# Performance work log

Hardware: AMD Instinct MI355X
Metric: run time of the kernel (lower is better)

The kernel has to match this reference:

```python
import jax, jax.numpy as jnp
import numpy as np

K = 3  # kernel_size
PAD = 1


def _unfold3x3(x):
    # x: [b, c, h, w] -> patches [b, c, k*k, h, w] matching torch.nn.Unfold
    # ordering (row-major over the kernel window, channel outermost).
    b, c, h, w = x.shape
    xp = jnp.pad(x, ((0, 0), (0, 0), (PAD, PAD), (PAD, PAD)))
    patches = jnp.stack(
        [xp[:, :, i:i + h, j:j + w] for i in range(K) for j in range(K)],
        axis=2,
    )
    return patches  # [b, c, 9, h, w]


def setup_inputs() -> dict:
    key = jax.random.key(0)
    k1, k2, k3, k4 = jax.random.split(key, 4)
    b, c, h, w = 8, 64, 128, 128
    out_ch = 64
    x = jax.random.normal(k1, (b, c, h, w), dtype=jnp.float32)
    guide_ch = jax.random.normal(k2, (b, c, h, w), dtype=jnp.float32)
    guide_sp = jax.random.normal(k3, (b, K * K, h, w), dtype=jnp.float32)
    # kaiming_normal_ fan_out on [out, in, k^2, 1, 1]: fan_out = out * k^2 * 1 * 1?
    # torch fan_out for 5D conv weight = out_channels * receptive_field (k^2*1*1)
    fan_out = out_ch * (K * K)
    std = np.sqrt(2.0 / fan_out)
    weight = jax.random.normal(k4, (out_ch, c, K * K), dtype=jnp.float32) * std
    return {"x": x, "guide_ch": guide_ch, "guide_sp": guide_sp, "weight": weight}


def reference(x, guide_ch, guide_sp, weight):
    # filter: [b, c, k^2, h, w] = 1 + tanh(guide_ch[:, :, None] + guide_sp[:, None])
    filt = 1.0 + jnp.tanh(guide_ch[:, :, None, :, :] + guide_sp[:, None, :, :, :])
    patches = _unfold3x3(x)  # [b, c, 9, h, w]
    # conv3d with weight [out, in, k^2, 1, 1] == per-pixel reduction over (c, k^2)
    out = jnp.einsum('bckhw,ock->bohw', patches * filt, weight)
    return out
```

## Files before the change

### kernel.cpp

```cpp
#include <hip/hip_runtime.h>
#include <hip/hip_bf16.h>

typedef short short8 __attribute__((ext_vector_type(8)));
typedef float floatx4 __attribute__((ext_vector_type(4)));

#define HWSZ 16384
#define WD 128
#define CD 64
#define OD 64
#define XSTR 72
#define OSTR 132
#define L2E2 2.8853900817779268f

__device__ __forceinline__ short f2bf(float f) {
    unsigned u = __builtin_bit_cast(unsigned, f);
    u += 0x7FFFu + ((u >> 16) & 1u);
    return (short)(u >> 16);
}

__device__ __forceinline__ unsigned pack2bf(float a, float b) {
    __hip_bfloat162 h = __float22bfloat162_rn(float2{a, b});
    unsigned u;
    __builtin_memcpy(&u, &h, 4);
    return u;
}

__device__ __forceinline__ float bf2f(short s) {
    return __builtin_bit_cast(float, ((unsigned)(unsigned short)s) << 16);
}

__global__ void prepack_w(const float* __restrict__ wgt, unsigned short* __restrict__ wp) {
    int idx = blockIdx.x * 256 + threadIdx.x;
    if (idx < 9 * 64 * 64) {
        int k = idx >> 12, o = (idx >> 6) & 63, c = idx & 63;
        wp[idx] = (unsigned short)f2bf(wgt[o * 576 + c * 9 + k]);
    }
}

__global__ __launch_bounds__(256, 3)
void paka_kernel(const float* __restrict__ x, const float* __restrict__ gc,
                 const float* __restrict__ gs, const float* __restrict__ wgt,
                 const unsigned short* __restrict__ wp, float* __restrict__ out)
{
    __shared__ union {
        struct {
            short xl[130 * XSTR];
            short wl[3][64 * XSTR];
        } s;
        float o[64 * OSTR];
    } lds;

    const int tid  = threadIdx.x;
    const int wave = tid >> 6;
    const int lane = tid & 63;
    const int b = blockIdx.x >> 7;
    const int h = blockIdx.x & 127;

    const float* xb  = x  + (size_t)b * CD * HWSZ;
    const float* gcb = gc + (size_t)b * CD * HWSZ;
    const float* gsb = gs + (size_t)b * 9 * HWSZ;

    const int row = lane & 15;
    const int q   = lane >> 4;
    const int mt0 = wave * 2;

    float eg[2][2][8];
    #pragma unroll
    for (int mt = 0; mt < 2; ++mt) {
        int p = (mt0 + mt) * 16 + row;
        #pragma unroll
        for (int ks = 0; ks < 2; ++ks)
            #pragma unroll
            for (int j = 0; j < 8; ++j) {
                int c = ks * 32 + q * 8 + j;
                eg[mt][ks][j] = __builtin_amdgcn_exp2f(gcb[(size_t)c * HWSZ + h * WD + p] * L2E2);
            }
    }
    float esv[9][2];
    #pragma unroll
    for (int k = 0; k < 9; ++k)
        #pragma unroll
        for (int mt = 0; mt < 2; ++mt) {
            int p = (mt0 + mt) * 16 + row;
            esv[k][mt] = __builtin_amdgcn_exp2f(gsb[k * HWSZ + h * WD + p] * L2E2);
        }

    if (tid < 32)
        *(unsigned*)&lds.s.xl[0 * XSTR + tid * 2] = 0u;
    else if (tid < 64)
        *(unsigned*)&lds.s.xl[129 * XSTR + (tid - 32) * 2] = 0u;

    floatx4 acc[2][4];
    #pragma unroll
    for (int i = 0; i < 2; ++i)
        #pragma unroll
        for (int n = 0; n < 4; ++n)
            acc[i][n] = (floatx4){0.f, 0.f, 0.f, 0.f};

    #pragma unroll
    for (int dh = 0; dh < 3; ++dh) {
        const int hh = h + dh - 1;
        if ((unsigned)hh >= 128u) continue;

        __syncthreads();

        if (wp) {
            #pragma unroll
            for (int it = 0; it < 6; ++it) {
                int idx = it * 256 + tid;
                int dw = idx >> 9, o = (idx >> 3) & 63, cg = idx & 7;
                short8 v = *(const short8*)&wp[(dh * 3 + dw) * 4096 + o * 64 + cg * 8];
                *(short8*)&lds.s.wl[dw][o * XSTR + cg * 8] = v;
            }
        } else {
            #pragma unroll
            for (int it = 0; it < 48; ++it) {
                int idx = it * 256 + tid;
                int dw = idx >> 12, o = (idx >> 6) & 63, c = idx & 63;
                lds.s.wl[dw][o * XSTR + c] = f2bf(wgt[o * 576 + c * 9 + dh * 3 + dw]);
            }
        }

        #pragma unroll
        for (int it = 0; it < 4; ++it) {
            int idx = it * 256 + tid;
            int cp = idx >> 5;
            int p4 = (idx & 31) * 4;
            const float* x0 = xb + (size_t)(2 * cp) * HWSZ + hh * WD + p4;
            floatx4 a = *(const floatx4*)x0;
            floatx4 c4 = *(const floatx4*)(x0 + HWSZ);
            #pragma unroll
            for (int i = 0; i < 4; ++i)
                *(unsigned*)&lds.s.xl[(p4 + i + 1) * XSTR + 2 * cp] = pack2bf(a[i], c4[i]);
        }

        __syncthreads();

        #pragma unroll
        for (int dw = 0; dw < 3; ++dw) {
            const int k = dh * 3 + dw;
            #pragma unroll
            for (int ks = 0; ks < 2; ++ks) {
                short8 af[2];
                #pragma unroll
                for (int mt = 0; mt < 2; ++mt) {
                    int wslot = (mt0 + mt) * 16 + row + dw;
                    short8 raw = *(const short8*)&lds.s.xl[wslot * XSTR + ks * 32 + q * 8];
                    float es = esv[k][mt];
                    #pragma unroll
                    for (int jj = 0; jj < 4; ++jj) {
                        float d0 = fmaf(eg[mt][ks][2 * jj],     es, 1.0f);
                        float d1 = fmaf(eg[mt][ks][2 * jj + 1], es, 1.0f);
                        float r0 = __builtin_amdgcn_rcpf(d0);
                        float r1 = __builtin_amdgcn_rcpf(d1);
                        float x20 = bf2f(raw[2 * jj]);     x20 += x20;
                        float x21 = bf2f(raw[2 * jj + 1]); x21 += x21;
                        float t0 = fmaf(-x20, r0, x20);
                        float t1 = fmaf(-x21, r1, x21);
                        ((unsigned*)&af[mt])[jj] = pack2bf(t0, t1);
                    }
                }
                #pragma unroll
                for (int nt = 0; nt < 4; ++nt) {
                    short8 bv = *(const short8*)&lds.s.wl[dw][(nt * 16 + row) * XSTR + ks * 32 + q * 8];
                    acc[0][nt] = __builtin_amdgcn_mfma_f32_16x16x32_bf16(af[0], bv, acc[0][nt], 0, 0, 0);
                    acc[1][nt] = __builtin_amdgcn_mfma_f32_16x16x32_bf16(af[1], bv, acc[1][nt], 0, 0, 0);
                }
            }
        }
    }

    __syncthreads();

    #pragma unroll
    for (int i = 0; i < 2; ++i) {
        int prow = (mt0 + i) * 16 + q * 4;
        #pragma unroll
        for (int nt = 0; nt < 4; ++nt) {
            int o = nt * 16 + row;
            #pragma unroll
            for (int r = 0; r < 4; ++r)
                lds.o[o * OSTR + prow + r] = acc[i][nt][r];
        }
    }

    __syncthreads();

    float* outb = out + ((size_t)b * OD) * HWSZ + h * WD;
    #pragma unroll
    for (int it = 0; it < 8; ++it) {
        int idx = it * 256 + tid;
        int o = idx >> 5, p4 = (idx & 31) * 4;
        *(floatx4*)&outb[(size_t)o * HWSZ + p4] = *(const floatx4*)&lds.o[o * OSTR + p4];
    }
}

extern "C" void kernel_launch(void* const* d_in, const int* in_sizes, int n_in,
                              void* d_out, int out_size, void* d_ws, size_t ws_size,
                              hipStream_t stream) {
    const float* x   = (const float*)d_in[0];
    const float* gcp = (const float*)d_in[1];
    const float* gsp = (const float*)d_in[2];
    const float* wgt = (const float*)d_in[3];
    float* out = (float*)d_out;

    const bool use_wp = ws_size >= (size_t)(9 * 64 * 64 * sizeof(unsigned short));
    unsigned short* wp = use_wp ? (unsigned short*)d_ws : nullptr;
    if (use_wp)
        prepack_w<<<dim3(144), dim3(256), 0, stream>>>(wgt, wp);
    paka_kernel<<<dim3(1024), dim3(256), 0, stream>>>(x, gcp, gsp, wgt, wp, out);
}
```

Baseline: 145.9 us.

## Pre-transpose x to padded bf16 NHWC and read operands directly from global

Adds a separate kernel that converts each input row of x into a zero-padded, channel-contiguous bf16 layout in workspace. The main kernel then loads A and B MFMA fragments straight from global/L2 instead of staging them through LDS, which removes the per-row syncthreads and shrinks LDS so occupancy can rise to 4 blocks. The factor of 2 is folded into the prepacked weights, and the spatial exponentials are computed per kernel row. This costs an extra kernel launch and an extra round trip of x through memory (about 33MB read, 17MB written), and it only runs when the workspace is large enough; otherwise a fallback kernel is used.

```diff
diff --git a/kernel.cpp b/kernel.cpp
--- a/kernel.cpp
+++ b/kernel.cpp
@@ -3,13 +3,15 @@
 
 typedef short short8 __attribute__((ext_vector_type(8)));
 typedef float floatx4 __attribute__((ext_vector_type(4)));
+typedef unsigned uint4v __attribute__((ext_vector_type(4)));
 
 #define HWSZ 16384
 #define WD 128
 #define CD 64
 #define OD 64
-#define XSTR 72
 #define OSTR 132
+#define XTROW (130 * 64)
+#define WP_BYTES (9 * 64 * 64 * 2)
 #define L2E2 2.8853900817779268f
 
 __device__ __forceinline__ short f2bf(float f) {
@@ -33,22 +35,52 @@
     int idx = blockIdx.x * 256 + threadIdx.x;
     if (idx < 9 * 64 * 64) {
         int k = idx >> 12, o = (idx >> 6) & 63, c = idx & 63;
-        wp[idx] = (unsigned short)f2bf(wgt[o * 576 + c * 9 + k]);
-    }
-}
-
-__global__ __launch_bounds__(256, 3)
-void paka_kernel(const float* __restrict__ x, const float* __restrict__ gc,
-                 const float* __restrict__ gs, const float* __restrict__ wgt,
-                 const unsigned short* __restrict__ wp, float* __restrict__ out)
+        wp[idx] = (unsigned short)f2bf(2.0f * wgt[o * 576 + c * 9 + k]);
+    }
+}
+
+__global__ __launch_bounds__(256, 2)
+void transpose_x(const float* __restrict__ x, unsigned short* __restrict__ xt) {
+    __shared__ unsigned ld[128 * 33];
+    const int tid = threadIdx.x;
+    const int b = blockIdx.x >> 7;
+    const int h = blockIdx.x & 127;
+    const float* xr = x + (size_t)b * CD * HWSZ + h * WD;
+
+    #pragma unroll
+    for (int it = 0; it < 16; ++it) {
+        int idx = it * 256 + tid;
+        int cd = idx >> 7;
+        int w  = idx & 127;
+        float a  = xr[(size_t)(2 * cd) * HWSZ + w];
+        float b2 = xr[(size_t)(2 * cd + 1) * HWSZ + w];
+        ld[w * 33 + cd] = pack2bf(a, b2);
+    }
+    __syncthreads();
+
+    unsigned short* xo = xt + (size_t)(b * 128 + h) * XTROW;
+    if (tid < 16) {
+        int slot = (tid >> 3) ? 129 : 0;
+        int cq = tid & 7;
+        *(uint4v*)&xo[slot * 64 + cq * 8] = (uint4v){0u, 0u, 0u, 0u};
+    }
+    #pragma unroll
+    for (int it = 0; it < 4; ++it) {
+        int idx = it * 256 + tid;
+        int w = idx >> 3, cq = idx & 7;
+        uint4v v;
+        #pragma unroll
+        for (int i = 0; i < 4; ++i) v[i] = ld[w * 33 + cq * 4 + i];
+        *(uint4v*)&xo[(1 + w) * 64 + cq * 8] = v;
+    }
+}
+
+__global__ __launch_bounds__(256, 4)
+void paka_main(const float* __restrict__ gc, const float* __restrict__ gs,
+               const unsigned short* __restrict__ wp,
+               const unsigned short* __restrict__ xt, float* __restrict__ out)
 {
-    __shared__ union {
-        struct {
-            short xl[130 * XSTR];
-            short wl[3][64 * XSTR];
-        } s;
-        float o[64 * OSTR];
-    } lds;
+    __shared__ float lo[64 * OSTR];
 
     const int tid  = threadIdx.x;
     const int wave = tid >> 6;
@@ -56,7 +88,6 @@
     const int b = blockIdx.x >> 7;
     const int h = blockIdx.x & 127;
 
-    const float* xb  = x  + (size_t)b * CD * HWSZ;
     const float* gcb = gc + (size_t)b * CD * HWSZ;
     const float* gsb = gs + (size_t)b * 9 * HWSZ;
 
@@ -76,19 +107,6 @@
                 eg[mt][ks][j] = __builtin_amdgcn_exp2f(gcb[(size_t)c * HWSZ + h * WD + p] * L2E2);
             }
     }
-    float esv[9][2];
-    #pragma unroll
-    for (int k = 0; k < 9; ++k)
-        #pragma unroll
-        for (int mt = 0; mt < 2; ++mt) {
-            int p = (mt0 + mt) * 16 + row;
-            esv[k][mt] = __builtin_amdgcn_exp2f(gsb[k * HWSZ + h * WD + p] * L2E2);
-        }
-
-    if (tid < 32)
-        *(unsigned*)&lds.s.xl[0 * XSTR + tid * 2] = 0u;
-    else if (tid < 64)
-        *(unsigned*)&lds.s.xl[129 * XSTR + (tid - 32) * 2] = 0u;
 
     floatx4 acc[2][4];
     #pragma unroll
@@ -102,30 +120,138 @@
         const int hh = h + dh - 1;
         if ((unsigned)hh >= 128u) continue;
 
+        const unsigned short* xr = xt + (size_t)(b * 128 + hh) * XTROW;
+
+        float esd[3][2];
+        #pragma unroll
+        for (int dw = 0; dw < 3; ++dw)
+            #pragma unroll
+            for (int mt = 0; mt < 2; ++mt) {
+                int p = (mt0 + mt) * 16 + row;
+                esd[dw][mt] = __builtin_amdgcn_exp2f(gsb[(dh * 3 + dw) * HWSZ + h * WD + p] * L2E2);
+            }
+
+        #pragma unroll
+        for (int dw = 0; dw < 3; ++dw) {
+            const int k = dh * 3 + dw;
+            #pragma unroll
+            for (int ks = 0; ks < 2; ++ks) {
+                short8 raw[2];
+                #pragma unroll
+                for (int mt = 0; mt < 2; ++mt) {
+                    int wslot = (mt0 + mt) * 16 + row + dw;
+                    raw[mt] = *(const short8*)&xr[(size_t)wslot * 64 + ks * 32 + q * 8];
+                }
+                short8 bv[4];
+                #pragma unroll
+                for (int nt = 0; nt < 4; ++nt)
+                    bv[nt] = *(const short8*)&wp[k * 4096 + (nt * 16 + row) * 64 + ks * 32 + q * 8];
+
+                short8 af[2];
+                #pragma unroll
+                for (int mt = 0; mt < 2; ++mt) {
+                    float es = esd[dw][mt];
+                    #pragma unroll
+                    for (int jj = 0; jj < 4; ++jj) {
+                        float d0 = fmaf(eg[mt][ks][2 * jj],     es, 1.0f);
+                        float d1 = fmaf(eg[mt][ks][2 * jj + 1], es, 1.0f);
+                        float r0 = __builtin_amdgcn_rcpf(d0);
+                        float r1 = __builtin_amdgcn_rcpf(d1);
+                        float x0 = bf2f(raw[mt][2 * jj]);
+                        float x1 = bf2f(raw[mt][2 * jj + 1]);
+                        float t0 = fmaf(-x0, r0, x0);
+                        float t1 = fmaf(-x1, r1, x1);
+                        ((unsigned*)&af[mt])[jj] = pack2bf(t0, t1);
+                    }
+                }
+                #pragma unroll
+                for (int nt = 0; nt < 4; ++nt) {
+                    acc[0][nt] = __builtin_amdgcn_mfma_f32_16x16x32_bf16(af[0], bv[nt], acc[0][nt], 0, 0, 0);
+                    acc[1][nt] = __builtin_amdgcn_mfma_f32_16x16x32_bf16(af[1], bv[nt], acc[1][nt], 0, 0, 0);
+                }
+            }
+        }
+    }
+
+    #pragma unroll
+    for (int i = 0; i < 2; ++i) {
+        int prow = (mt0 + i) * 16 + q * 4;
+        #pragma unroll
+        for (int nt = 0; nt < 4; ++nt) {
+            int o = nt * 16 + row;
+            #pragma unroll
+            for (int r = 0; r < 4; ++r)
+                lo[o * OSTR + prow + r] = acc[i][nt][r];
+        }
+    }
+    __syncthreads();
+
+    float* outb = out + ((size_t)b * OD) * HWSZ + h * WD;
+    #pragma unroll
+    for (int it = 0; it < 8; ++it) {
+        int idx = it * 256 + tid;
+        int o = idx >> 5, p4 = (idx & 31) * 4;
+        *(floatx4*)&outb[(size_t)o * HWSZ + p4] = *(const floatx4*)&lo[o * OSTR + p4];
+    }
+}
+
+#define XSTR 72
+__global__ __launch_bounds__(256, 3)
+void paka_fallback(const float* __restrict__ x, const float* __restrict__ gc,
+                   const float* __restrict__ gs, const float* __restrict__ wgt,
+                   float* __restrict__ out)
+{
+    __shared__ union {
+        struct { short xl[130 * XSTR]; short wl[3][64 * XSTR]; } s;
+        float o[64 * OSTR];
+    } lds;
+    const int tid  = threadIdx.x;
+    const int wave = tid >> 6;
+    const int lane = tid & 63;
+    const int b = blockIdx.x >> 7;
+    const int h = blockIdx.x & 127;
+    const float* xb  = x  + (size_t)b * CD * HWSZ;
+    const float* gcb = gc + (size_t)b * CD * HWSZ;
+    const float* gsb = gs + (size_t)b * 9 * HWSZ;
+    const int row = lane & 15, q = lane >> 4, mt0 = wave * 2;
+    float eg[2][2][8];
+    #pragma unroll
+    for (int mt = 0; mt < 2; ++mt) {
+        int p = (mt0 + mt) * 16 + row;
+        #pragma unroll
+        for (int ks = 0; ks < 2; ++ks)
+            #pragma unroll
+            for (int j = 0; j < 8; ++j)
+                eg[mt][ks][j] = __builtin_amdgcn_exp2f(gcb[(size_t)(ks * 32 + q * 8 + j) * HWSZ + h * WD + p] * L2E2);
+    }
+    float esv[9][2];
+    #pragma unroll
+    for (int k = 0; k < 9; ++k)
+        #pragma unroll
+        for (int mt = 0; mt < 2; ++mt)
+            esv[k][mt] = __builtin_amdgcn_exp2f(gsb[k * HWSZ + h * WD + (mt0 + mt) * 16 + row] * L2E2);
+    if (tid < 32) *(unsigned*)&lds.s.xl[0 * XSTR + tid * 2] = 0u;
+    else if (tid < 64) *(unsigned*)&lds.s.xl[129 * XSTR + (tid - 32) * 2] = 0u;
+    floatx4 acc[2][4];
+    #pragma unroll
+    for (int i = 0; i < 2; ++i)
+        #pragma unroll
+        for (int n = 0; n < 4; ++n) acc[i][n] = (floatx4){0.f, 0.f, 0.f, 0.f};
+    #pragma unroll
+    for (int dh = 0; dh < 3; ++dh) {
+        const int hh = h + dh - 1;
+        if ((unsigned)hh >= 128u) continue;
         __syncthreads();
-
-        if (wp) {
-            #pragma unroll
-            for (int it = 0; it < 6; ++it) {
-                int idx = it * 256 + tid;
-                int dw = idx >> 9, o = (idx >> 3) & 63, cg = idx & 7;
-                short8 v = *(const short8*)&wp[(dh * 3 + dw) * 4096 + o * 64 + cg * 8];
-                *(short8*)&lds.s.wl[dw][o * XSTR + cg * 8] = v;
-            }
-        } else {
-            #pragma unroll
-            for (int it = 0; it < 48; ++it) {
-                int idx = it * 256 + tid;
-                int dw = idx >> 12, o = (idx >> 6) & 63, c = idx & 63;
-                lds.s.wl[dw][o * XSTR + c] = f2bf(wgt[o * 576 + c * 9 + dh * 3 + dw]);
-            }
-        }
-
+        #pragma unroll
+        for (int it = 0; it < 48; ++it) {
+            int idx = it * 256 + tid;
+            int dw = idx >> 12, o = (idx >> 6) & 63, c = idx & 63;
+            lds.s.wl[dw][o * XSTR + c] = f2bf(wgt[o * 576 + c * 9 + dh * 3 + dw]);
+        }
         #pragma unroll
         for (int it = 0; it < 4; ++it) {
             int idx = it * 256 + tid;
-            int cp = idx >> 5;
-            int p4 = (idx & 31) * 4;
+            int cp = idx >> 5, p4 = (idx & 31) * 4;
             const float* x0 = xb + (size_t)(2 * cp) * HWSZ + hh * WD + p4;
             floatx4 a = *(const floatx4*)x0;
             floatx4 c4 = *(const floatx4*)(x0 + HWSZ);
@@ -133,9 +259,7 @@
             for (int i = 0; i < 4; ++i)
                 *(unsigned*)&lds.s.xl[(p4 + i + 1) * XSTR + 2 * cp] = pack2bf(a[i], c4[i]);
         }
-
         __syncthreads();
-
         #pragma unroll
         for (int dw = 0; dw < 3; ++dw) {
             const int k = dh * 3 + dw;
@@ -169,9 +293,7 @@
             }
         }
     }
-
     __syncthreads();
-
     #pragma unroll
     for (int i = 0; i < 2; ++i) {
         int prow = (mt0 + i) * 16 + q * 4;
@@ -183,9 +305,7 @@
                 lds.o[o * OSTR + prow + r] = acc[i][nt][r];
         }
     }
-
     __syncthreads();
-
     float* outb = out + ((size_t)b * OD) * HWSZ + h * WD;
     #pragma unroll
     for (int it = 0; it < 8; ++it) {
@@ -204,9 +324,15 @@
     const float* wgt = (const float*)d_in[3];
     float* out = (float*)d_out;
 
-    const bool use_wp = ws_size >= (size_t)(9 * 64 * 64 * sizeof(unsigned short));
-    unsigned short* wp = use_wp ? (unsigned short*)d_ws : nullptr;
-    if (use_wp)
+    const size_t xt_bytes = (size_t)8 * 128 * XTROW * 2;
+    const size_t need = WP_BYTES + xt_bytes;
+    if (ws_size >= need) {
+        unsigned short* wp = (unsigned short*)d_ws;
+        unsigned short* xt = (unsigned short*)((char*)d_ws + WP_BYTES);
         prepack_w<<<dim3(144), dim3(256), 0, stream>>>(wgt, wp);
-    paka_kernel<<<dim3(1024), dim3(256), 0, stream>>>(x, gcp, gsp, wgt, wp, out);
-}
+        transpose_x<<<dim3(1024), dim3(256), 0, stream>>>(x, xt);
+        paka_main<<<dim3(1024), dim3(256), 0, stream>>>(gcp, gsp, wp, xt, out);
+    } else {
+        paka_fallback<<<dim3(1024), dim3(256), 0, stream>>>(x, gcp, gsp, wgt, out);
+    }
+}
```

After: 164.2 us. +12.6%, slower.
